# Kernel tuning notes

Hardware: AMD Instinct MI355X
Metric: run time of the kernel (lower is better)

## Reference

```python
import jax, jax.numpy as jnp
import numpy as np


def setup_inputs() -> dict:
    key = jax.random.key(0)
    ks = jax.random.split(key, 8)
    B, S, H = 32, 2048, 1024
    scale = 1.0 / np.sqrt(H)
    return {
        "query": jax.random.normal(ks[0], (B, H), jnp.float32),
        "keys": jax.random.normal(ks[1], (B, S, H), jnp.float32),
        "Wa_w": jax.random.normal(ks[2], (H, H), jnp.float32) * scale,
        "Wa_b": jax.random.normal(ks[3], (H,), jnp.float32) * scale,
        "Ua_w": jax.random.normal(ks[4], (H, H), jnp.float32) * scale,
        "Ua_b": jax.random.normal(ks[5], (H,), jnp.float32) * scale,
        "Va_w": jax.random.normal(ks[6], (1, H), jnp.float32) * scale,
        "Va_b": jax.random.normal(ks[7], (1,), jnp.float32) * scale,
    }


def reference(query, keys, Wa_w, Wa_b, Ua_w, Ua_b, Va_w, Va_b):
    # q_proj: [B, H] -> broadcast over S instead of repeat
    q_proj = query @ Wa_w.T + Wa_b              # [B, H]
    k_proj = jnp.einsum("bsh,oh->bso", keys, Ua_w) + Ua_b  # [B, S, H]
    e = jnp.tanh(q_proj[:, None, :] + k_proj)   # [B, S, H]
    scores = jnp.einsum("bsh,h->bs", e, Va_w[0]) + Va_b[0]  # [B, S]
    weights = jax.nn.softmax(scores, axis=-1)   # [B, S]
    context = jnp.einsum("bs,bsh->bh", weights, keys)       # [B, H]
    return (context, weights)
```

## Files before the change

kernel.cpp:

```cpp
#include <hip/hip_runtime.h>
#include <hip/hip_bf16.h>
#include <cstdint>


typedef short s8v __attribute__((ext_vector_type(8)));
typedef float f4v __attribute__((ext_vector_type(4)));

static __device__ __forceinline__ unsigned short f2bf(float f) {
  union { float f; uint32_t u; } x; x.f = f;
  uint32_t u = x.u;
  return (unsigned short)((u + 0x7FFFu + ((u >> 16) & 1u)) >> 16);
}
static __device__ __forceinline__ float bf2f(unsigned short u) {
  union { float f; uint32_t u; } x; x.u = ((uint32_t)u) << 16; return x.f;
}
static __device__ __forceinline__ float fast_tanh(float x) {
  float e2 = __expf(2.0f * x);
  return 1.0f - 2.0f / (e2 + 1.0f);
}

#define GLL16(src, dst)                                                        \
  __builtin_amdgcn_global_load_lds(                                            \
      (const __attribute__((address_space(1))) void*)(src),                    \
      (__attribute__((address_space(3))) void*)(dst), 16, 0, 0)

#define WAITV(n) asm volatile("s_waitcnt vmcnt(" #n ")" ::: "memory")

__global__ void cvt_kernel(const float* __restrict__ in, unsigned short* __restrict__ out, int n8) {
  int i = blockIdx.x * blockDim.x + threadIdx.x;
  int step = gridDim.x * blockDim.x;
  for (; i < n8; i += step) {
    const float4* p = (const float4*)(in + (size_t)i * 8);
    float4 a = p[0], b = p[1];
    union { unsigned short us[8]; uint4 v; } o;
    o.us[0] = f2bf(a.x); o.us[1] = f2bf(a.y); o.us[2] = f2bf(a.z); o.us[3] = f2bf(a.w);
    o.us[4] = f2bf(b.x); o.us[5] = f2bf(b.y); o.us[6] = f2bf(b.z); o.us[7] = f2bf(b.w);
    ((uint4*)out)[i] = o.v;
  }
}

__global__ void qproj_kernel(const float* __restrict__ query, const float* __restrict__ Wa_w,
                             const float* __restrict__ Wa_b, const float* __restrict__ Ua_b,
                             float* __restrict__ qp) {
  int b = blockIdx.x, oc = blockIdx.y;
  __shared__ float qsh[1024];
  for (int i = threadIdx.x; i < 1024; i += 256) qsh[i] = query[b * 1024 + i];
  __syncthreads();
  int wid = threadIdx.x >> 6, lane = threadIdx.x & 63;
  const float4* q4 = (const float4*)qsh;
  for (int it = 0; it < 16; ++it) {
    int o = oc * 64 + it * 4 + wid;
    const float4* row = (const float4*)(Wa_w + (size_t)o * 1024);
    float s = 0.f;
#pragma unroll
    for (int j = 0; j < 4; ++j) {
      float4 w = row[j * 64 + lane];
      float4 q = q4[j * 64 + lane];
      s += w.x * q.x + w.y * q.y + w.z * q.z + w.w * q.w;
    }
#pragma unroll
    for (int m = 32; m; m >>= 1) s += __shfl_xor(s, m, 64);
    if (lane == 0) qp[b * 1024 + o] = s + Wa_b[o] + Ua_b[o];
  }
}

__global__ __launch_bounds__(256, 4) void gemm_score_sb(
    const unsigned short* __restrict__ keys_bf,
    const unsigned short* __restrict__ ua_bf,
    const float* __restrict__ qp, const float* __restrict__ va,
    float* __restrict__ scores) {
  __shared__ unsigned short ldsA[128 * 64];
  __shared__ unsigned short ldsB[128 * 64];

  int bid = blockIdx.x;
  int wg  = (bid & 7) * 512 + (bid >> 3);
  int mt  = wg >> 3;
  int nt  = wg & 7;
  int t   = threadIdx.x;
  int wid = t >> 6, lane = t & 63;
  int wm = wid >> 1, wn = wid & 1;
  int lr = lane & 15, lk = lane >> 4;

  f4v acc[4][4];
#pragma unroll
  for (int mi = 0; mi < 4; ++mi)
#pragma unroll
    for (int ni = 0; ni < 4; ++ni) acc[mi][ni] = (f4v){0.f, 0.f, 0.f, 0.f};

  const unsigned short* srcA[4];
  const unsigned short* srcB[4];
  int dstOff[4];
#pragma unroll
  for (int i = 0; i < 4; ++i) {
    int u = i * 256 + t;
    int r = u >> 3;
    int c = (u & 7) ^ (r & 7);
    srcA[i] = keys_bf + (size_t)(mt * 128 + r) * 1024 + c * 8;
    srcB[i] = ua_bf  + (size_t)(nt * 128 + r) * 1024 + c * 8;
    dstOff[i] = u * 8;
  }

  int offA[2][4], offB[2][4];
#pragma unroll
  for (int kk = 0; kk < 2; ++kk) {
#pragma unroll
    for (int mi = 0; mi < 4; ++mi)
      offA[kk][mi] = (wm * 64 + mi * 16 + lr) * 64 + (((kk * 4 + lk) ^ (lr & 7)) * 8);
#pragma unroll
    for (int ni = 0; ni < 4; ++ni)
      offB[kk][ni] = (wn * 64 + ni * 16 + lr) * 64 + (((kk * 4 + lk) ^ (lr & 7)) * 8);
  }

  for (int kt = 0; kt < 16; ++kt) {
#pragma unroll
    for (int i = 0; i < 4; ++i) {
      GLL16(srcA[i] + kt * 64, ldsA + dstOff[i]);
      GLL16(srcB[i] + kt * 64, ldsB + dstOff[i]);
    }
    WAITV(0);
    __syncthreads();
#pragma unroll
    for (int kk = 0; kk < 2; ++kk) {
      s8v a[4], b[4];
#pragma unroll
      for (int mi = 0; mi < 4; ++mi) a[mi] = *(const s8v*)(ldsA + offA[kk][mi]);
#pragma unroll
      for (int ni = 0; ni < 4; ++ni) b[ni] = *(const s8v*)(ldsB + offB[kk][ni]);
#pragma unroll
      for (int mi = 0; mi < 4; ++mi)
#pragma unroll
        for (int ni = 0; ni < 4; ++ni)
          acc[mi][ni] = __builtin_amdgcn_mfma_f32_16x16x32_bf16(a[mi], b[ni], acc[mi][ni], 0, 0, 0);
    }
    __syncthreads();
  }

  int b = mt >> 4;
  float qv[4], vv[4];
#pragma unroll
  for (int ni = 0; ni < 4; ++ni) {
    int o = nt * 128 + wn * 64 + ni * 16 + lr;
    qv[ni] = qp[b * 1024 + o];
    vv[ni] = va[o];
  }
#pragma unroll
  for (int mi = 0; mi < 4; ++mi) {
#pragma unroll
    for (int r = 0; r < 4; ++r) {
      float sum = 0.f;
#pragma unroll
      for (int ni = 0; ni < 4; ++ni)
        sum += vv[ni] * fast_tanh(acc[mi][ni][r] + qv[ni]);
      sum += __shfl_xor(sum, 1, 64);
      sum += __shfl_xor(sum, 2, 64);
      sum += __shfl_xor(sum, 4, 64);
      sum += __shfl_xor(sum, 8, 64);
      if (lr == 0)
        atomicAdd(&scores[(size_t)mt * 128 + wm * 64 + mi * 16 + lk * 4 + r], sum);
    }
  }
}

__global__ __launch_bounds__(256, 2) void gemm_score_fallback(
    const float* __restrict__ keys_f, const unsigned short* __restrict__ ua_bf,
    const float* __restrict__ qp, const float* __restrict__ va,
    float* __restrict__ scores) {
  __shared__ unsigned short ldsA[2][128 * 64];
  __shared__ unsigned short ldsB[2][128 * 64];
  int bid = blockIdx.x;
  int wg  = (bid & 7) * 512 + (bid >> 3);
  int mt  = wg >> 3, nt = wg & 7;
  int t   = threadIdx.x;
  int wid = t >> 6, lane = t & 63;
  int wm = wid >> 1, wn = wid & 1;
  int lr = lane & 15, lk = lane >> 4;
  f4v acc[4][4];
#pragma unroll
  for (int mi = 0; mi < 4; ++mi)
#pragma unroll
    for (int ni = 0; ni < 4; ++ni) acc[mi][ni] = (f4v){0.f, 0.f, 0.f, 0.f};
  int colb = (t & 7) * 8;
  auto stage = [&](int kt, int buf) {
#pragma unroll
    for (int i = 0; i < 4; ++i) {
      int flat = i * 256 + t;
      int row  = flat >> 3;
      const float4* src = (const float4*)(keys_f + (size_t)(mt * 128 + row) * 1024 + kt * 64 + colb);
      float4 a = src[0], c = src[1];
      union { unsigned short us[8]; s8v v; } o;
      o.us[0] = f2bf(a.x); o.us[1] = f2bf(a.y); o.us[2] = f2bf(a.z); o.us[3] = f2bf(a.w);
      o.us[4] = f2bf(c.x); o.us[5] = f2bf(c.y); o.us[6] = f2bf(c.z); o.us[7] = f2bf(c.w);
      *(s8v*)&ldsA[buf][flat * 8] = o.v;
      const unsigned short* srcB = ua_bf + (size_t)(nt * 128 + row) * 1024 + kt * 64 + colb;
      GLL16(srcB, &ldsB[buf][flat * 8]);
    }
  };
  auto compute = [&](int buf) {
#pragma unroll
    for (int kk = 0; kk < 2; ++kk) {
      s8v af[4], bfr[4];
#pragma unroll
      for (int mi = 0; mi < 4; ++mi)
        af[mi] = *(const s8v*)&ldsA[buf][(wm * 64 + mi * 16 + lr) * 64 + kk * 32 + lk * 8];
#pragma unroll
      for (int ni = 0; ni < 4; ++ni)
        bfr[ni] = *(const s8v*)&ldsB[buf][(wn * 64 + ni * 16 + lr) * 64 + kk * 32 + lk * 8];
#pragma unroll
      for (int mi = 0; mi < 4; ++mi)
#pragma unroll
        for (int ni = 0; ni < 4; ++ni)
          acc[mi][ni] = __builtin_amdgcn_mfma_f32_16x16x32_bf16(af[mi], bfr[ni], acc[mi][ni], 0, 0, 0);
    }
  };
  stage(0, 0);
  for (int kt = 0; kt < 16; ++kt) {
    __syncthreads();
    if (kt + 1 < 16) stage(kt + 1, (kt + 1) & 1);
    compute(kt & 1);
  }
  int b = mt >> 4;
  float qv[4], vv[4];
#pragma unroll
  for (int ni = 0; ni < 4; ++ni) {
    int o = nt * 128 + wn * 64 + ni * 16 + lr;
    qv[ni] = qp[b * 1024 + o];
    vv[ni] = va[o];
  }
#pragma unroll
  for (int mi = 0; mi < 4; ++mi) {
#pragma unroll
    for (int r = 0; r < 4; ++r) {
      float sum = 0.f;
#pragma unroll
      for (int ni = 0; ni < 4; ++ni)
        sum += vv[ni] * fast_tanh(acc[mi][ni][r] + qv[ni]);
      sum += __shfl_xor(sum, 1, 64);
      sum += __shfl_xor(sum, 2, 64);
      sum += __shfl_xor(sum, 4, 64);
      sum += __shfl_xor(sum, 8, 64);
      if (lr == 0)
        atomicAdd(&scores[(size_t)mt * 128 + wm * 64 + mi * 16 + lk * 4 + r], sum);
    }
  }
}

__global__ void softmax_kernel(const float* __restrict__ scores, float* __restrict__ w) {
  int b = blockIdx.x, t = threadIdx.x;
  int wid = t >> 6, lane = t & 63;
  __shared__ float redm[4], reds[4];
  const float4* src = (const float4*)(scores + b * 2048 + t * 8);
  float4 x = src[0], y = src[1];
  float v[8] = {x.x, x.y, x.z, x.w, y.x, y.y, y.z, y.w};
  float mx = v[0];
#pragma unroll
  for (int j = 1; j < 8; ++j) mx = fmaxf(mx, v[j]);
#pragma unroll
  for (int m = 32; m; m >>= 1) mx = fmaxf(mx, __shfl_xor(mx, m, 64));
  if (lane == 0) redm[wid] = mx;
  __syncthreads();
  mx = fmaxf(fmaxf(redm[0], redm[1]), fmaxf(redm[2], redm[3]));
  float e[8], s = 0.f;
#pragma unroll
  for (int j = 0; j < 8; ++j) { e[j] = __expf(v[j] - mx); s += e[j]; }
#pragma unroll
  for (int m = 32; m; m >>= 1) s += __shfl_xor(s, m, 64);
  if (lane == 0) reds[wid] = s;
  __syncthreads();
  float inv = 1.f / (reds[0] + reds[1] + reds[2] + reds[3]);
  float4 o0 = {e[0] * inv, e[1] * inv, e[2] * inv, e[3] * inv};
  float4 o1 = {e[4] * inv, e[5] * inv, e[6] * inv, e[7] * inv};
  float4* dst = (float4*)(w + b * 2048 + t * 8);
  dst[0] = o0; dst[1] = o1;
}

template<bool KBF>
__global__ void context_kernel(const unsigned short* __restrict__ keys_bf,
                               const float* __restrict__ keys_f,
                               const float* __restrict__ w, float* __restrict__ ctx) {
  int b = blockIdx.y, sc = blockIdx.x, t = threadIdx.x;
  int h = t * 4;
  float a0 = 0, a1 = 0, a2 = 0, a3 = 0;
  for (int s0 = 0; s0 < 64; ++s0) {
    int s = sc * 64 + s0;
    float ws = w[b * 2048 + s];
    if constexpr (KBF) {
      ushort4 kv = *(const ushort4*)(keys_bf + ((size_t)(b * 2048 + s)) * 1024 + h);
      a0 += ws * bf2f(kv.x); a1 += ws * bf2f(kv.y);
      a2 += ws * bf2f(kv.z); a3 += ws * bf2f(kv.w);
    } else {
      float4 kv = *(const float4*)(keys_f + ((size_t)(b * 2048 + s)) * 1024 + h);
      a0 += ws * kv.x; a1 += ws * kv.y; a2 += ws * kv.z; a3 += ws * kv.w;
    }
  }
  atomicAdd(&ctx[b * 1024 + h + 0], a0);
  atomicAdd(&ctx[b * 1024 + h + 1], a1);
  atomicAdd(&ctx[b * 1024 + h + 2], a2);
  atomicAdd(&ctx[b * 1024 + h + 3], a3);
}

extern "C" void kernel_launch(void* const* d_in, const int* in_sizes, int n_in,
                              void* d_out, int out_size, void* d_ws, size_t ws_size,
                              hipStream_t stream) {
  const float* query = (const float*)d_in[0];
  const float* keys  = (const float*)d_in[1];
  const float* Wa_w  = (const float*)d_in[2];
  const float* Wa_b  = (const float*)d_in[3];
  const float* Ua_w  = (const float*)d_in[4];
  const float* Ua_b  = (const float*)d_in[5];
  const float* Va_w  = (const float*)d_in[6];

  float* out = (float*)d_out;
  float* ctx = out;
  float* wts = out + 32768;

  char* ws = (char*)d_ws;
  unsigned short* ua_bf   = (unsigned short*)ws;
  float*          qp      = (float*)(ws + 2 * 1024 * 1024);
  float*          scores  = (float*)(ws + 2 * 1024 * 1024 + 131072);
  unsigned short* keys_bf = (unsigned short*)(ws + 2 * 1024 * 1024 + 131072 + 262144);
  const size_t need_big = 2ull * 1024 * 1024 + 131072 + 262144 + 67108864ull * 2;
  bool big = ws_size >= need_big;

  hipMemsetAsync(scores, 0, 65536 * 4, stream);
  hipMemsetAsync(ctx, 0, 32768 * 4, stream);

  cvt_kernel<<<512, 256, 0, stream>>>(Ua_w, ua_bf, 1048576 / 8);
  if (big) cvt_kernel<<<2048, 256, 0, stream>>>(keys, keys_bf, 67108864 / 8);

  qproj_kernel<<<dim3(32, 16), 256, 0, stream>>>(query, Wa_w, Wa_b, Ua_b, qp);

  if (big) gemm_score_sb<<<4096, 256, 0, stream>>>(keys_bf, ua_bf, qp, Va_w, scores);
  else     gemm_score_fallback<<<4096, 256, 0, stream>>>(keys, ua_bf, qp, Va_w, scores);

  softmax_kernel<<<32, 256, 0, stream>>>(scores, wts);

  if (big) context_kernel<true ><<<dim3(32, 32), 256, 0, stream>>>(keys_bf, nullptr, wts, ctx);
  else     context_kernel<false><<<dim3(32, 32), 256, 0, stream>>>(nullptr, keys, wts, ctx);
}
```

Baseline: 292.2 us.

## Enlarge score GEMM tile to 256x256 with 8 waves and double-buffered LDS

Replaces the 128x128 single-buffered score GEMM with a 256x256 tile run by 512 threads (8 waves, each computing 128x64). LDS is double-buffered so the global-to-LDS load for step kt+2 is issued while step kt computes, with partial vmcnt waits and setprio around the MFMA bursts. The larger tile halves global traffic per FLOP and the prefetch hides load latency. In exchange it uses 128 KB of LDS, more accumulator registers, and fewer, larger workgroups.

Result: slower. 317.7 us (+8.7%).

```diff
diff --git a/kernel.cpp b/kernel.cpp
--- a/kernel.cpp
+++ b/kernel.cpp
@@ -25,6 +25,12 @@
       (__attribute__((address_space(3))) void*)(dst), 16, 0, 0)
 
 #define WAITV(n) asm volatile("s_waitcnt vmcnt(" #n ")" ::: "memory")
+#define BARRIER()                                                              \
+  do {                                                                         \
+    __builtin_amdgcn_s_barrier();                                              \
+    asm volatile("" ::: "memory");                                             \
+    __builtin_amdgcn_sched_barrier(0);                                         \
+  } while (0)
 
 __global__ void cvt_kernel(const float* __restrict__ in, unsigned short* __restrict__ out, int n8) {
   int i = blockIdx.x * blockDim.x + threadIdx.x;
@@ -64,26 +70,26 @@
   }
 }
 
-__global__ __launch_bounds__(256, 4) void gemm_score_sb(
+__global__ __launch_bounds__(512, 2) void gemm_score_8p(
     const unsigned short* __restrict__ keys_bf,
     const unsigned short* __restrict__ ua_bf,
     const float* __restrict__ qp, const float* __restrict__ va,
     float* __restrict__ scores) {
-  __shared__ unsigned short ldsA[128 * 64];
-  __shared__ unsigned short ldsB[128 * 64];
+  __shared__ unsigned short ldsA[2][256 * 64];
+  __shared__ unsigned short ldsB[2][256 * 64];
 
   int bid = blockIdx.x;
-  int wg  = (bid & 7) * 512 + (bid >> 3);
-  int mt  = wg >> 3;
-  int nt  = wg & 7;
+  int wg  = (bid & 7) * 128 + (bid >> 3);
+  int mt  = wg >> 2;
+  int nt  = wg & 3;
   int t   = threadIdx.x;
   int wid = t >> 6, lane = t & 63;
-  int wm = wid >> 1, wn = wid & 1;
-  int lr = lane & 15, lk = lane >> 4;
-
-  f4v acc[4][4];
-#pragma unroll
-  for (int mi = 0; mi < 4; ++mi)
+  int wr  = wid >> 2, wc = wid & 3;
+  int lr  = lane & 15, lk = lane >> 4;
+
+  f4v acc[8][4];
+#pragma unroll
+  for (int mi = 0; mi < 8; ++mi)
 #pragma unroll
     for (int ni = 0; ni < 4; ++ni) acc[mi][ni] = (f4v){0.f, 0.f, 0.f, 0.f};
 
@@ -92,59 +98,82 @@
   int dstOff[4];
 #pragma unroll
   for (int i = 0; i < 4; ++i) {
-    int u = i * 256 + t;
+    int u = i * 512 + t;
     int r = u >> 3;
     int c = (u & 7) ^ (r & 7);
-    srcA[i] = keys_bf + (size_t)(mt * 128 + r) * 1024 + c * 8;
-    srcB[i] = ua_bf  + (size_t)(nt * 128 + r) * 1024 + c * 8;
+    srcA[i] = keys_bf + (size_t)(mt * 256 + r) * 1024 + c * 8;
+    srcB[i] = ua_bf  + (size_t)(nt * 256 + r) * 1024 + c * 8;
     dstOff[i] = u * 8;
   }
 
-  int offA[2][4], offB[2][4];
-#pragma unroll
-  for (int kk = 0; kk < 2; ++kk) {
-#pragma unroll
-    for (int mi = 0; mi < 4; ++mi)
-      offA[kk][mi] = (wm * 64 + mi * 16 + lr) * 64 + (((kk * 4 + lk) ^ (lr & 7)) * 8);
-#pragma unroll
-    for (int ni = 0; ni < 4; ++ni)
-      offB[kk][ni] = (wn * 64 + ni * 16 + lr) * 64 + (((kk * 4 + lk) ^ (lr & 7)) * 8);
-  }
+  auto stage = [&](int kt) {
+    unsigned short* bA = &ldsA[kt & 1][0];
+    unsigned short* bB = &ldsB[kt & 1][0];
+    int go = kt * 64;
+#pragma unroll
+    for (int i = 0; i < 4; ++i) {
+      GLL16(srcA[i] + go, bA + dstOff[i]);
+      GLL16(srcB[i] + go, bB + dstOff[i]);
+    }
+  };
+
+  int swz[2];
+  swz[0] = ((lk ^ (lr & 7)) * 8);
+  swz[1] = (((4 + lk) ^ (lr & 7)) * 8);
+  int rowA[8], rowB[4];
+#pragma unroll
+  for (int mi = 0; mi < 8; ++mi) rowA[mi] = (wr * 128 + mi * 16 + lr) * 64;
+#pragma unroll
+  for (int ni = 0; ni < 4; ++ni) rowB[ni] = (wc * 64 + ni * 16 + lr) * 64;
+
+  auto compute = [&](int kt) {
+    const unsigned short* bA = &ldsA[kt & 1][0];
+    const unsigned short* bB = &ldsB[kt & 1][0];
+#pragma unroll
+    for (int kk = 0; kk < 2; ++kk) {
+      s8v b[4];
+#pragma unroll
+      for (int ni = 0; ni < 4; ++ni) b[ni] = *(const s8v*)(bB + rowB[ni] + swz[kk]);
+#pragma unroll
+      for (int mh = 0; mh < 2; ++mh) {
+        s8v a[4];
+#pragma unroll
+        for (int j = 0; j < 4; ++j) a[j] = *(const s8v*)(bA + rowA[mh * 4 + j] + swz[kk]);
+        asm volatile("s_waitcnt lgkmcnt(0)" ::: "memory");
+        __builtin_amdgcn_sched_barrier(0);
+        __builtin_amdgcn_s_setprio(1);
+#pragma unroll
+        for (int j = 0; j < 4; ++j)
+#pragma unroll
+          for (int ni = 0; ni < 4; ++ni)
+            acc[mh * 4 + j][ni] =
+                __builtin_amdgcn_mfma_f32_16x16x32_bf16(a[j], b[ni], acc[mh * 4 + j][ni], 0, 0, 0);
+        __builtin_amdgcn_s_setprio(0);
+      }
+    }
+  };
+
+  stage(0); stage(1);
 
   for (int kt = 0; kt < 16; ++kt) {
-#pragma unroll
-    for (int i = 0; i < 4; ++i) {
-      GLL16(srcA[i] + kt * 64, ldsA + dstOff[i]);
-      GLL16(srcB[i] + kt * 64, ldsB + dstOff[i]);
-    }
-    WAITV(0);
-    __syncthreads();
-#pragma unroll
-    for (int kk = 0; kk < 2; ++kk) {
-      s8v a[4], b[4];
-#pragma unroll
-      for (int mi = 0; mi < 4; ++mi) a[mi] = *(const s8v*)(ldsA + offA[kk][mi]);
-#pragma unroll
-      for (int ni = 0; ni < 4; ++ni) b[ni] = *(const s8v*)(ldsB + offB[kk][ni]);
-#pragma unroll
-      for (int mi = 0; mi < 4; ++mi)
-#pragma unroll
-        for (int ni = 0; ni < 4; ++ni)
-          acc[mi][ni] = __builtin_amdgcn_mfma_f32_16x16x32_bf16(a[mi], b[ni], acc[mi][ni], 0, 0, 0);
-    }
-    __syncthreads();
-  }
-
-  int b = mt >> 4;
+    if (kt < 15) WAITV(8);
+    else WAITV(0);
+    BARRIER();
+    compute(kt);
+    BARRIER();
+    if (kt + 2 < 16) stage(kt + 2);
+  }
+
+  int b = mt >> 3;
   float qv[4], vv[4];
 #pragma unroll
   for (int ni = 0; ni < 4; ++ni) {
-    int o = nt * 128 + wn * 64 + ni * 16 + lr;
+    int o = nt * 256 + wc * 64 + ni * 16 + lr;
     qv[ni] = qp[b * 1024 + o];
     vv[ni] = va[o];
   }
 #pragma unroll
-  for (int mi = 0; mi < 4; ++mi) {
+  for (int mi = 0; mi < 8; ++mi) {
 #pragma unroll
     for (int r = 0; r < 4; ++r) {
       float sum = 0.f;
@@ -156,7 +185,7 @@
       sum += __shfl_xor(sum, 4, 64);
       sum += __shfl_xor(sum, 8, 64);
       if (lr == 0)
-        atomicAdd(&scores[(size_t)mt * 128 + wm * 64 + mi * 16 + lk * 4 + r], sum);
+        atomicAdd(&scores[(size_t)mt * 256 + wr * 128 + mi * 16 + lk * 4 + r], sum);
     }
   }
 }
@@ -329,7 +358,7 @@
 
   qproj_kernel<<<dim3(32, 16), 256, 0, stream>>>(query, Wa_w, Wa_b, Ua_b, qp);
 
-  if (big) gemm_score_sb<<<4096, 256, 0, stream>>>(keys_bf, ua_bf, qp, Va_w, scores);
+  if (big) gemm_score_8p<<<1024, 512, 0, stream>>>(keys_bf, ua_bf, qp, Va_w, scores);
   else     gemm_score_fallback<<<4096, 256, 0, stream>>>(keys, ua_bf, qp, Va_w, scores);
 
   softmax_kernel<<<32, 256, 0, stream>>>(scores, wts);
```
